# Performance work log

Hardware: AMD Instinct MI355X
Metric: run time of the kernel (lower is better)

Reference implementation:

```python
import jax, jax.numpy as jnp
import numpy as np

EPS = 1e-5  # torch BatchNorm1d default eps

# BinActive: sign forward, straight-through estimator backward (grad clipped where |x|>1)
@jax.custom_vjp
def bin_active(x):
    return jnp.sign(x)

def _ba_fwd(x):
    return jnp.sign(x), x

def _ba_bwd(x, g):
    return (g * (jnp.abs(x) <= 1.0).astype(g.dtype),)

bin_active.defvjp(_ba_fwd, _ba_bwd)

# XNOR-style weight binarization: sign(W) * mean(|W|) per output column, STE backward
@jax.custom_vjp
def bin_weight(w):
    alpha = jnp.mean(jnp.abs(w), axis=0, keepdims=True)  # [1, out]
    return jnp.sign(w) * alpha

def _bw_fwd(w):
    alpha = jnp.mean(jnp.abs(w), axis=0, keepdims=True)
    return jnp.sign(w) * alpha, w

def _bw_bwd(w, g):
    return (g * (jnp.abs(w) <= 1.0).astype(g.dtype),)

bin_weight.defvjp(_bw_fwd, _bw_bwd)


def setup_inputs() -> dict:
    key = jax.random.key(0)
    ks = jax.random.split(key, 8)
    N, E, IN, H, OUT = 100000, 1600000, 256, 128, 40
    x = jax.random.normal(ks[0], (N, IN), dtype=jnp.float32)
    edge_index = jax.random.randint(ks[1], (2, E), 0, N, dtype=jnp.int64)
    W0 = jax.random.normal(ks[2], (IN, H), dtype=jnp.float32) * (2.0 / IN) ** 0.5
    b0 = jnp.zeros((H,), dtype=jnp.float32)
    W1 = jax.random.normal(ks[3], (H, H), dtype=jnp.float32) * (2.0 / H) ** 0.5
    b1 = jnp.zeros((H,), dtype=jnp.float32)
    W2 = jax.random.normal(ks[4], (H, OUT), dtype=jnp.float32) * (2.0 / H) ** 0.5
    b2 = jnp.zeros((OUT,), dtype=jnp.float32)
    return {"x": x, "edge_index": edge_index, "W0": W0, "b0": b0,
            "W1": W1, "b1": b1, "W2": W2, "b2": b2}


def reference(x, edge_index, W0, b0, W1, b1, W2, b2):
    n = x.shape[0]
    loop = jnp.arange(n, dtype=edge_index.dtype)
    src = jnp.concatenate([edge_index[0], loop])  # add self loops (GCN norm)
    dst = jnp.concatenate([edge_index[1], loop])
    deg = jax.ops.segment_sum(jnp.ones_like(src, dtype=x.dtype), dst, num_segments=n)
    dinv = jnp.where(deg > 0, deg ** -0.5, 0.0)
    norm = (dinv[src] * dinv[dst])[:, None]  # [E+N, 1]

    # BatchNorm1d(affine=False), training-mode batch statistics (biased var)
    mu = jnp.mean(x, axis=0)
    var = jnp.var(x, axis=0)
    h = (x - mu) * jax.lax.rsqrt(var + EPS)

    for W, b in ((W0, b0), (W1, b1), (W2, b2)):
        h = bin_active(h)                       # sign binarize (dropout skipped: eval)
        h = h @ bin_weight(W)                   # binary-weight linear
        h = jax.ops.segment_sum(h[src] * norm, dst, num_segments=n) + b  # D^-1/2 (A+I) D^-1/2 agg
    return jax.nn.log_softmax(h, axis=1)
```

## Files before the change

### kernel.cpp

```cpp
#include <hip/hip_runtime.h>
#include <math.h>

#define IN_DIM 256
#define HD 128
#define OUT_DIM 40
#define S2_STRIDE 64
#define NB_CS 1024
#define NXCD 8
#define NCHUNK 64
#define NRANGE 4
#define RMAXW 6400

__device__ __forceinline__ int xcc_id() {
    int x;
    asm volatile("s_getreg_b32 %0, hwreg(HW_REG_XCC_ID)" : "=s"(x));
    return x & (NXCD - 1);
}

__device__ __forceinline__ void nt_load4(const int* p, int* o) {
    o[0] = __builtin_nontemporal_load(p + 0);
    o[1] = __builtin_nontemporal_load(p + 1);
    o[2] = __builtin_nontemporal_load(p + 2);
    o[3] = __builtin_nontemporal_load(p + 3);
}

__global__ __launch_bounds__(256) void k_init(float* muacc8) {
    int i = blockIdx.x * 256 + threadIdx.x;
    if (i < NXCD * 256) muacc8[i] = 0.f;
}

__global__ __launch_bounds__(256) void k_fuse1(const float* __restrict__ x, int N,
                                               float* __restrict__ muacc8,
                                               const int* __restrict__ ei, int E,
                                               unsigned char* __restrict__ cntC,
                                               const float* __restrict__ W0,
                                               const float* __restrict__ W1,
                                               const float* __restrict__ W2,
                                               unsigned long long* W0p,
                                               unsigned long long* W1p,
                                               unsigned long long* W2p,
                                               float* aS0, float* aS1, float* aS2) {
    __shared__ __align__(16) unsigned ldsbuf[RMAXW];
    int b = blockIdx.x, tid = threadIdx.x;
    if (b < NB_CS) {
        float* lds = (float*)ldsbuf;
        size_t F4 = (size_t)N * (IN_DIM / 4);
        size_t stride = (size_t)NB_CS * 256;
        float a0 = 0.f, a1 = 0.f, a2 = 0.f, a3 = 0.f;
        const float4* x4 = (const float4*)x;
        for (size_t i = (size_t)b * 256 + tid; i < F4; i += stride) {
            float4 v = x4[i];
            a0 += v.x; a1 += v.y; a2 += v.z; a3 += v.w;
        }
        lds[tid] = 0.f;
        __syncthreads();
        int c0 = (tid * 4) & 255;
        atomicAdd(&lds[c0], a0);
        atomicAdd(&lds[c0 + 1], a1);
        atomicAdd(&lds[c0 + 2], a2);
        atomicAdd(&lds[c0 + 3], a3);
        __syncthreads();
        int xc = xcc_id();
        __hip_atomic_fetch_add(&muacc8[xc * 256 + tid], lds[tid],
                               __ATOMIC_RELAXED, __HIP_MEMORY_SCOPE_WORKGROUP);
    } else if (b < NB_CS + NCHUNK * NRANGE) {
        int bid2 = b - NB_CS;
        int c = bid2 >> 2, r = bid2 & (NRANGE - 1);
        for (int i = tid; i < RMAXW; i += 256) ldsbuf[i] = 0u;
        __syncthreads();
        int R = (N + NRANGE - 1) / NRANGE;
        int base = r * R;
        int lim = N - base; if (lim > R) lim = R; if (lim < 0) lim = 0;
        int chunk = ((E + NCHUNK - 1) / NCHUNK + 3) & ~3;
        int eBeg = c * chunk, eEnd = E < eBeg + chunk ? E : eBeg + chunk;
        const int* dptr = ei + E;
        int e = eBeg;
        if ((((unsigned)(E + eBeg)) & 3u) == 0 && eBeg < eEnd) {
            int n4 = (eEnd - eBeg) >> 2;
            for (int i = tid; i < n4; i += 256) {
                int dd[4];
                nt_load4(dptr + eBeg + 4 * i, dd);
                unsigned r0 = (unsigned)(dd[0] - base);
                unsigned r1 = (unsigned)(dd[1] - base);
                unsigned r2 = (unsigned)(dd[2] - base);
                unsigned r3 = (unsigned)(dd[3] - base);
                if (r0 < (unsigned)lim) atomicAdd(&ldsbuf[r0 >> 2], 1u << (8 * (r0 & 3)));
                if (r1 < (unsigned)lim) atomicAdd(&ldsbuf[r1 >> 2], 1u << (8 * (r1 & 3)));
                if (r2 < (unsigned)lim) atomicAdd(&ldsbuf[r2 >> 2], 1u << (8 * (r2 & 3)));
                if (r3 < (unsigned)lim) atomicAdd(&ldsbuf[r3 >> 2], 1u << (8 * (r3 & 3)));
            }
            e = eBeg + (n4 << 2);
        }
        for (e += tid; e < eEnd; e += 256) {
            unsigned rel = (unsigned)(dptr[e] - base);
            if (rel < (unsigned)lim) atomicAdd(&ldsbuf[rel >> 2], 1u << (8 * (rel & 3)));
        }
        __syncthreads();
        for (int i = tid; i < lim; i += 256) {
            unsigned cv = (ldsbuf[i >> 2] >> (8 * (i & 3))) & 0xFFu;
            cntC[(size_t)c * N + base + i] = (unsigned char)cv;
        }
    } else {
        int b2 = b - NB_CS - NCHUNK * NRANGE;
        int lane = tid & 63, w = tid >> 6;
        if (b2 < 32) {
            int j = b2 * 4 + w;
            float asum = 0.f;
            unsigned long long words[4];
            #pragma unroll
            for (int q = 0; q < 4; ++q) {
                float v = W0[(size_t)(4 * lane + q) * HD + j];
                asum += fabsf(v);
                words[q] = __ballot(v < 0.f);
            }
            #pragma unroll
            for (int off = 32; off; off >>= 1) asum += __shfl_xor(asum, off);
            if (lane == 0) {
                aS0[j] = 2.f * asum / 256.f;
                #pragma unroll
                for (int q = 0; q < 4; ++q) W0p[j * 4 + q] = words[q];
            }
        } else if (b2 < 64) {
            int j = (b2 - 32) * 4 + w;
            float asum = 0.f;
            unsigned long long words[2];
            #pragma unroll
            for (int p = 0; p < 2; ++p) {
                float v = W1[(size_t)(2 * lane + p) * HD + j];
                asum += fabsf(v);
                words[p] = __ballot(v < 0.f);
            }
            #pragma unroll
            for (int off = 32; off; off >>= 1) asum += __shfl_xor(asum, off);
            if (lane == 0) {
                aS1[j] = 2.f * asum / 128.f;
                W1p[j * 2 + 0] = words[0];
                W1p[j * 2 + 1] = words[1];
            }
        } else {
            int j = (b2 - 64) * 4 + w;
            if (j < OUT_DIM) {
                float asum = 0.f;
                unsigned long long words[2];
                #pragma unroll
                for (int p = 0; p < 2; ++p) {
                    float v = W2[(size_t)(2 * lane + p) * OUT_DIM + j];
                    asum += fabsf(v);
                    words[p] = __ballot(v < 0.f);
                }
                #pragma unroll
                for (int off = 32; off; off >>= 1) asum += __shfl_xor(asum, off);
                if (lane == 0) {
                    aS2[j] = 2.f * asum / 128.f;
                    W2p[j * 2 + 0] = words[0];
                    W2p[j * 2 + 1] = words[1];
                }
            }
        }
    }
}

__global__ __launch_bounds__(256) void k_bp(unsigned char* __restrict__ cntC, int N,
                                            int* bp, float* __restrict__ dinv,
                                            int* __restrict__ cnt) {
    __shared__ int sm[256];
    int i = blockIdx.x * 256 + threadIdx.x;
    int c = 0;
    if (i < N) {
        int run = 0;
        #pragma unroll
        for (int h = 0; h < NCHUNK; ++h) {
            unsigned bc = cntC[(size_t)h * N + i];
            cntC[(size_t)h * N + i] = (unsigned char)run;
            run += (int)bc;
        }
        c = run;
        cnt[i] = run;
        dinv[i] = (float)(1.0 / sqrt((double)(run + 1)));
    }
    sm[threadIdx.x] = c;
    __syncthreads();
    for (int off = 128; off; off >>= 1) {
        if (threadIdx.x < off) sm[threadIdx.x] += sm[threadIdx.x + off];
        __syncthreads();
    }
    if (threadIdx.x == 0) bp[blockIdx.x] = sm[0];
}

__global__ __launch_bounds__(512) void k_scanbp(const int* __restrict__ bp, int NB, int* bps,
                                                const float* __restrict__ muacc8,
                                                float* __restrict__ mu) {
    __shared__ int sm[512];
    int t = threadIdx.x;
    if (t < 256) {
        float s = 0.f;
        #pragma unroll
        for (int xc = 0; xc < NXCD; ++xc) s += muacc8[xc * 256 + t];
        mu[t] = s;
    }
    int v = (t < NB) ? bp[t] : 0;
    sm[t] = v;
    __syncthreads();
    for (int off = 1; off < 512; off <<= 1) {
        int add = (t >= off) ? sm[t - off] : 0;
        __syncthreads();
        sm[t] += add;
        __syncthreads();
    }
    if (t < NB) bps[t] = sm[t] - v;
}

__global__ __launch_bounds__(256) void k_rowptr(const int* __restrict__ cnt,
                                                const int* __restrict__ bps, int N, int E,
                                                int* row_ptr) {
    __shared__ int wsum[4];
    int t = threadIdx.x, lane = t & 63, w = t >> 6;
    int i = blockIdx.x * 256 + t;
    int c = (i < N) ? cnt[i] : 0;
    int v = c;
    #pragma unroll
    for (int off = 1; off < 64; off <<= 1) {
        int n = __shfl_up(v, off);
        if (lane >= off) v += n;
    }
    if (lane == 63) wsum[w] = v;
    __syncthreads();
    int wo = 0;
    for (int k = 0; k < w; ++k) wo += wsum[k];
    int excl = bps[blockIdx.x] + wo + v - c;
    if (i < N) row_ptr[i] = excl;
    if (blockIdx.x == 0 && t == 0) row_ptr[N] = E;
}

__global__ __launch_bounds__(256) void k_fuse2(const int* __restrict__ ei, int E,
                                               const int* __restrict__ rowp,
                                               const unsigned char* __restrict__ xoffC,
                                               int* __restrict__ cs4,
                                               const float* __restrict__ x,
                                               const float* __restrict__ muacc, float inv_n,
                                               const unsigned long long* __restrict__ W0p,
                                               unsigned char* __restrict__ S0, int N) {
    __shared__ __align__(16) unsigned sh32[RMAXW];
    int b = blockIdx.x, tid = threadIdx.x;
    if (b < NCHUNK * NRANGE) {
        int c = b >> 2, r = b & (NRANGE - 1);
        for (int i = tid; i < RMAXW; i += 256) sh32[i] = 0u;
        __syncthreads();
        int R = (N + NRANGE - 1) / NRANGE;
        int base = r * R;
        int lim = N - base; if (lim > R) lim = R; if (lim < 0) lim = 0;
        int chunk = ((E + NCHUNK - 1) / NCHUNK + 3) & ~3;
        int eBeg = c * chunk, eEnd = E < eBeg + chunk ? E : eBeg + chunk;
        int e = eBeg;
        if (((unsigned)eBeg & 3u) == 0 && (((unsigned)(E + eBeg)) & 3u) == 0 && eBeg < eEnd) {
            int n4 = (eEnd - eBeg) >> 2;
            for (int i = tid; i < n4; i += 256) {
                int ss[4], dd[4];
                nt_load4(ei + eBeg + 4 * i, ss);
                nt_load4(ei + E + eBeg + 4 * i, dd);
                #pragma unroll
                for (int k = 0; k < 4; ++k) {
                    unsigned rel = (unsigned)(dd[k] - base);
                    if (rel < (unsigned)lim) {
                        unsigned old = atomicAdd(&sh32[rel >> 2], 1u << (8 * (rel & 3)));
                        int lr = (int)((old >> (8 * (rel & 3))) & 0xFFu);
                        int pos = rowp[dd[k]] +
                                  (int)xoffC[(size_t)c * N + dd[k]] + lr;
                        cs4[pos] = ss[k];
                    }
                }
            }
            e = eBeg + (n4 << 2);
        }
        for (e += tid; e < eEnd; e += 256) {
            int d = ei[E + e];
            unsigned rel = (unsigned)(d - base);
            if (rel < (unsigned)lim) {
                unsigned old = atomicAdd(&sh32[rel >> 2], 1u << (8 * (rel & 3)));
                int lr = (int)((old >> (8 * (rel & 3))) & 0xFFu);
                int pos = rowp[d] + (int)xoffC[(size_t)c * N + d] + lr;
                cs4[pos] = ei[e];
            }
        }
    } else {
        unsigned long long* w0s = (unsigned long long*)sh32;
        {
            int i = tid;
            w0s[9 * (i >> 3) + (i & 7)] = W0p[i];
            i = tid + 256;
            w0s[9 * (i >> 3) + (i & 7)] = W0p[i];
        }
        __syncthreads();
        int lane = tid & 63;
        int row = (b - NCHUNK * NRANGE) * 4 + (tid >> 6);
        if (row >= N) return;
        float4 xv = ((const float4*)(x + (size_t)row * IN_DIM))[lane];
        float4 ms = ((const float4*)muacc)[lane];
        unsigned long long xw[4];
        xw[0] = __ballot(xv.x < ms.x * inv_n);
        xw[1] = __ballot(xv.y < ms.y * inv_n);
        xw[2] = __ballot(xv.z < ms.z * inv_n);
        xw[3] = __ballot(xv.w < ms.w * inv_n);
        unsigned int pack = 0;
        #pragma unroll
        for (int t2 = 0; t2 < 2; ++t2) {
            const unsigned long long* wc = &w0s[9 * lane + 4 * t2];
            int dd = __popcll(xw[0] ^ wc[0]) + __popcll(xw[1] ^ wc[1]) +
                     __popcll(xw[2] ^ wc[2]) + __popcll(xw[3] ^ wc[3]);
            int S = IN_DIM - 2 * dd;
            int s8 = S >> 1;
            if (s8 > 127) s8 = 127;
            pack |= ((unsigned int)(s8 + 128) & 0xffu) << (8 * t2);
        }
        *(unsigned short*)(S0 + (size_t)row * HD + 2 * lane) = (unsigned short)pack;
    }
}

template <int OUTC>
__global__ __launch_bounds__(256) void k_agg_mm(const unsigned char* __restrict__ Sin,
                                                const int* __restrict__ row_ptr,
                                                const int* __restrict__ cs4,
                                                const float* __restrict__ dinv,
                                                const float* __restrict__ alphaS,
                                                const float* __restrict__ bias,
                                                const unsigned long long* __restrict__ Wnp,
                                                unsigned char* __restrict__ Sout, int N) {
    __shared__ unsigned long long wsm[OUTC * 2 + OUTC / 4 + 8];
    int tid = threadIdx.x;
    for (int i = tid; i < OUTC * 2; i += 256) wsm[9 * (i >> 3) + (i & 7)] = Wnp[i];
    __syncthreads();
    int lane = tid & 63;
    int d = blockIdx.x * 4 + (tid >> 6);
    if (d >= N) return;
    unsigned fo = (unsigned)lane * 2;
    float dv = dinv[d];
    float p0a[4] = {0.f, 0.f, 0.f, 0.f};
    float p1a[4] = {0.f, 0.f, 0.f, 0.f};
    {
        float nrm = dv * dv;
        unsigned v = *(const unsigned short*)(Sin + (((unsigned)d << 7) + fo));
        p0a[0] = fmaf(nrm, (float)(v & 0xffu) - 128.f, p0a[0]);
        p1a[0] = fmaf(nrm, (float)(v >> 8) - 128.f, p1a[0]);
    }
    int e0 = row_ptr[d], e1 = row_ptr[d + 1];
    int e = e0;
    for (; e + 7 < e1; e += 8) {
        int s[8]; float n[8]; unsigned v[8];
        #pragma unroll
        for (int j = 0; j < 8; ++j) s[j] = __builtin_nontemporal_load(&cs4[e + j]);
        #pragma unroll
        for (int j = 0; j < 8; ++j) n[j] = dinv[s[j]] * dv;
        #pragma unroll
        for (int j = 0; j < 8; ++j)
            v[j] = *(const unsigned short*)(Sin + (((unsigned)s[j] << 7) + fo));
        #pragma unroll
        for (int j = 0; j < 8; ++j) {
            p0a[j & 3] = fmaf(n[j], (float)(v[j] & 0xffu) - 128.f, p0a[j & 3]);
            p1a[j & 3] = fmaf(n[j], (float)(v[j] >> 8) - 128.f, p1a[j & 3]);
        }
    }
    for (int q = 0; e < e1; ++e, ++q) {
        int s = cs4[e];
        float nrm = dinv[s] * dv;
        unsigned v = *(const unsigned short*)(Sin + (((unsigned)s << 7) + fo));
        p0a[q & 3] = fmaf(nrm, (float)(v & 0xffu) - 128.f, p0a[q & 3]);
        p1a[q & 3] = fmaf(nrm, (float)(v >> 8) - 128.f, p1a[q & 3]);
    }
    float a0 = (p0a[0] + p0a[1]) + (p0a[2] + p0a[3]);
    float a1 = (p1a[0] + p1a[1]) + (p1a[2] + p1a[3]);
    float h0 = alphaS[fo] * a0 + bias[fo];
    float h1 = alphaS[fo + 1] * a1 + bias[fo + 1];
    unsigned long long x0 = __ballot(h0 < 0.f);
    unsigned long long x1 = __ballot(h1 < 0.f);
    if (OUTC == 128) {
        unsigned pack = 0;
        #pragma unroll
        for (int t2 = 0; t2 < 2; ++t2) {
            int j = 2 * lane + t2;
            int i0 = j * 2;
            const unsigned long long* wc = &wsm[9 * (i0 >> 3) + (i0 & 7)];
            int dd = __popcll(x0 ^ wc[0]) + __popcll(x1 ^ wc[1]);
            int S = HD - 2 * dd;
            pack |= ((unsigned)((S >> 1) + 128) & 0xffu) << (8 * t2);
        }
        *(unsigned short*)(Sout + (size_t)d * HD + fo) = (unsigned short)pack;
    } else {
        int p8 = 128;
        if (lane < OUTC) {
            int i0 = lane * 2;
            const unsigned long long* wc = &wsm[9 * (i0 >> 3) + (i0 & 7)];
            int dd = __popcll(x0 ^ wc[0]) + __popcll(x1 ^ wc[1]);
            p8 = ((HD - 2 * dd) >> 1) + 128;
        }
        Sout[(size_t)d * S2_STRIDE + lane] = (unsigned char)p8;
    }
}

__global__ __launch_bounds__(256) void k_agg_out(const unsigned char* __restrict__ S2,
                                                 const int* __restrict__ row_ptr,
                                                 const int* __restrict__ cs4,
                                                 const float* __restrict__ dinv,
                                                 const float* __restrict__ alphaS2,
                                                 const float* __restrict__ b2,
                                                 float* __restrict__ out, int N) {
    int tid = threadIdx.x, lane = tid & 63;
    int d = blockIdx.x * 4 + (tid >> 6);
    if (d >= N) return;
    float dv = dinv[d];
    float pa[4] = {0.f, 0.f, 0.f, 0.f};
    {
        float nrm = dv * dv;
        unsigned v = S2[((unsigned)d << 6) + lane];
        pa[0] = fmaf(nrm, (float)v - 128.f, pa[0]);
    }
    int e0 = row_ptr[d], e1 = row_ptr[d + 1];
    int e = e0;
    for (; e + 7 < e1; e += 8) {
        int s[8]; float n[8]; unsigned v[8];
        #pragma unroll
        for (int j = 0; j < 8; ++j) s[j] = __builtin_nontemporal_load(&cs4[e + j]);
        #pragma unroll
        for (int j = 0; j < 8; ++j) n[j] = dinv[s[j]] * dv;
        #pragma unroll
        for (int j = 0; j < 8; ++j) v[j] = S2[((unsigned)s[j] << 6) + lane];
        #pragma unroll
        for (int j = 0; j < 8; ++j) pa[j & 3] = fmaf(n[j], (float)v[j] - 128.f, pa[j & 3]);
    }
    for (int q = 0; e < e1; ++e, ++q) {
        int s = cs4[e];
        float nrm = dinv[s] * dv;
        unsigned v = S2[((unsigned)s << 6) + lane];
        pa[q & 3] = fmaf(nrm, (float)v - 128.f, pa[q & 3]);
    }
    float a0 = (pa[0] + pa[1]) + (pa[2] + pa[3]);
    float h = (lane < OUT_DIM) ? (alphaS2[lane] * a0 + b2[lane]) : -INFINITY;
    float mymax = h;
    #pragma unroll
    for (int off = 1; off < 64; off <<= 1) mymax = fmaxf(mymax, __shfl_xor(mymax, off));
    float s4 = (lane < OUT_DIM) ? expf(h - mymax) : 0.f;
    #pragma unroll
    for (int off = 1; off < 64; off <<= 1) s4 += __shfl_xor(s4, off);
    float lse = mymax + logf(s4);
    if (lane < OUT_DIM) out[(size_t)d * OUT_DIM + lane] = h - lse;
}

extern "C" void kernel_launch(void* const* d_in, const int* in_sizes, int n_in,
                              void* d_out, int out_size, void* d_ws, size_t ws_size,
                              hipStream_t stream) {
    const float* x  = (const float*)d_in[0];
    const int*   ei = (const int*)d_in[1];
    const float* W0 = (const float*)d_in[2];
    const float* b0 = (const float*)d_in[3];
    const float* W1 = (const float*)d_in[4];
    const float* b1 = (const float*)d_in[5];
    const float* W2 = (const float*)d_in[6];
    const float* b2 = (const float*)d_in[7];
    float* out = (float*)d_out;

    int N = in_sizes[0] / IN_DIM;
    int E = in_sizes[1] / 2;

    char* ws = (char*)d_ws;
    size_t off = 0;
    auto alloc = [&](size_t bytes) -> void* {
        off = (off + 255) & ~(size_t)255;
        void* p = (void*)(ws + off);
        off += bytes;
        return p;
    };
    float* mu     = (float*)alloc(256 * 4);
    float* muacc8 = (float*)alloc(NXCD * 256 * 4);
    unsigned char* cntC = (unsigned char*)alloc((size_t)NCHUNK * N);
    int*   cnt    = (int*)alloc((size_t)N * 4);
    float* dinv   = (float*)alloc((size_t)N * 4);
    int*   rowp   = (int*)alloc(((size_t)N + 1) * 4);
    int*   bp     = (int*)alloc(512 * 4);
    int*   bps    = (int*)alloc(512 * 4);
    int*   cs4    = (int*)alloc((size_t)E * 4);
    unsigned char* S0 = (unsigned char*)alloc((size_t)N * HD);
    unsigned char* S1 = (unsigned char*)alloc((size_t)N * HD);
    unsigned char* S2 = (unsigned char*)alloc((size_t)N * S2_STRIDE);
    unsigned long long* W0p = (unsigned long long*)alloc(128 * 4 * 8);
    unsigned long long* W1p = (unsigned long long*)alloc(128 * 2 * 8);
    unsigned long long* W2p = (unsigned long long*)alloc(40 * 2 * 8);
    float* aS0 = (float*)alloc(128 * 4);
    float* aS1 = (float*)alloc(128 * 4);
    float* aS2 = (float*)alloc(40 * 4);

    int nb256 = (N + 255) / 256;
    float inv_n = 1.0f / (float)N;

    k_init<<<dim3(8), dim3(256), 0, stream>>>(muacc8);
    k_fuse1<<<dim3(NB_CS + NCHUNK * NRANGE + 74), dim3(256), 0, stream>>>(
        x, N, muacc8, ei, E, cntC, W0, W1, W2, W0p, W1p, W2p, aS0, aS1, aS2);
    k_bp<<<dim3(nb256), dim3(256), 0, stream>>>(cntC, N, bp, dinv, cnt);
    k_scanbp<<<dim3(1), dim3(512), 0, stream>>>(bp, nb256, bps, muacc8, mu);
    k_rowptr<<<dim3(nb256), dim3(256), 0, stream>>>(cnt, bps, N, E, rowp);

    int nb4 = (N + 3) / 4;
    k_fuse2<<<dim3(NCHUNK * NRANGE + nb4), dim3(256), 0, stream>>>(
        ei, E, rowp, cntC, cs4, x, mu, inv_n, W0p, S0, N);
    k_agg_mm<128><<<dim3(nb4), dim3(256), 0, stream>>>(S0, rowp, cs4, dinv, aS0, b0, W1p, S1, N);
    k_agg_mm<40><<<dim3(nb4), dim3(256), 0, stream>>>(S1, rowp, cs4, dinv, aS1, b1, W2p, S2, N);
    k_agg_out<<<dim3(nb4), dim3(256), 0, stream>>>(S2, rowp, cs4, dinv, aS2, b2, out, N);
    (void)out_size; (void)ws_size; (void)n_in;
}
```

Before: 536.2 us.

## Split aggregation wave across edges with 16-byte row loads and shuffle reduction

The aggregation kernels now assign sub-groups of lanes to different edges. In the hidden layers, 8 edge slots of 8 lanes each load 16-byte chunks of int8 rows. In the output layer, 16 slots of 4 lanes each do the same. Partial sums are then reduced across slots with shuffles. Previously every lane read 2 bytes per edge in a sequential edge loop. The sign bits are rebuilt through per-bit ballots, and the weight packing order in k_fuse1 is permuted to match the new feature-to-lane mapping. The aim is fewer, wider gathers and more edges in flight per wave, at the cost of 16 accumulators per lane plus extra shuffle and ballot work.

```diff
diff --git a/kernel.cpp b/kernel.cpp
--- a/kernel.cpp
+++ b/kernel.cpp
@@ -22,6 +22,18 @@
     o[1] = __builtin_nontemporal_load(p + 1);
     o[2] = __builtin_nontemporal_load(p + 2);
     o[3] = __builtin_nontemporal_load(p + 3);
+}
+
+__device__ __forceinline__ void addrow16(float n, uint4 r, float* acc) {
+    unsigned w[4] = {r.x, r.y, r.z, r.w};
+    #pragma unroll
+    for (int q = 0; q < 4; ++q) {
+        unsigned v = w[q];
+        acc[4 * q + 0] = fmaf(n, (float)(v & 0xffu) - 128.f, acc[4 * q + 0]);
+        acc[4 * q + 1] = fmaf(n, (float)((v >> 8) & 0xffu) - 128.f, acc[4 * q + 1]);
+        acc[4 * q + 2] = fmaf(n, (float)((v >> 16) & 0xffu) - 128.f, acc[4 * q + 2]);
+        acc[4 * q + 3] = fmaf(n, (float)(v >> 24) - 128.f, acc[4 * q + 3]);
+    }
 }
 
 __global__ __launch_bounds__(256) void k_init(float* muacc8) {
@@ -122,11 +134,12 @@
             }
         } else if (b2 < 64) {
             int j = (b2 - 32) * 4 + w;
+            int row0 = (lane & 7) * 16 + (lane >> 3);
             float asum = 0.f;
             unsigned long long words[2];
             #pragma unroll
             for (int p = 0; p < 2; ++p) {
-                float v = W1[(size_t)(2 * lane + p) * HD + j];
+                float v = W1[(size_t)(row0 + 8 * p) * HD + j];
                 asum += fabsf(v);
                 words[p] = __ballot(v < 0.f);
             }
@@ -139,12 +152,13 @@
             }
         } else {
             int j = (b2 - 64) * 4 + w;
+            int row0 = (lane & 7) * 16 + (lane >> 3);
             if (j < OUT_DIM) {
                 float asum = 0.f;
                 unsigned long long words[2];
                 #pragma unroll
                 for (int p = 0; p < 2; ++p) {
-                    float v = W2[(size_t)(2 * lane + p) * OUT_DIM + j];
+                    float v = W2[(size_t)(row0 + 8 * p) * OUT_DIM + j];
                     asum += fabsf(v);
                     words[p] = __ballot(v < 0.f);
                 }
@@ -332,46 +346,53 @@
     int lane = tid & 63;
     int d = blockIdx.x * 4 + (tid >> 6);
     if (d >= N) return;
-    unsigned fo = (unsigned)lane * 2;
+    int slot = lane >> 3;
+    unsigned fo = ((unsigned)lane & 7) * 16;
     float dv = dinv[d];
-    float p0a[4] = {0.f, 0.f, 0.f, 0.f};
-    float p1a[4] = {0.f, 0.f, 0.f, 0.f};
-    {
+    float acc[16];
+    #pragma unroll
+    for (int k = 0; k < 16; ++k) acc[k] = 0.f;
+    if (slot == 0) {
         float nrm = dv * dv;
-        unsigned v = *(const unsigned short*)(Sin + (((unsigned)d << 7) + fo));
-        p0a[0] = fmaf(nrm, (float)(v & 0xffu) - 128.f, p0a[0]);
-        p1a[0] = fmaf(nrm, (float)(v >> 8) - 128.f, p1a[0]);
+        uint4 r = *(const uint4*)(Sin + (((size_t)d) << 7) + fo);
+        addrow16(nrm, r, acc);
     }
     int e0 = row_ptr[d], e1 = row_ptr[d + 1];
-    int e = e0;
-    for (; e + 7 < e1; e += 8) {
-        int s[8]; float n[8]; unsigned v[8];
-        #pragma unroll
-        for (int j = 0; j < 8; ++j) s[j] = __builtin_nontemporal_load(&cs4[e + j]);
-        #pragma unroll
-        for (int j = 0; j < 8; ++j) n[j] = dinv[s[j]] * dv;
-        #pragma unroll
-        for (int j = 0; j < 8; ++j)
-            v[j] = *(const unsigned short*)(Sin + (((unsigned)s[j] << 7) + fo));
-        #pragma unroll
-        for (int j = 0; j < 8; ++j) {
-            p0a[j & 3] = fmaf(n[j], (float)(v[j] & 0xffu) - 128.f, p0a[j & 3]);
-            p1a[j & 3] = fmaf(n[j], (float)(v[j] >> 8) - 128.f, p1a[j & 3]);
-        }
-    }
-    for (int q = 0; e < e1; ++e, ++q) {
+    int e = e0 + slot;
+    for (; e + 8 < e1; e += 16) {
+        int sA = cs4[e], sB = cs4[e + 8];
+        float nA = dinv[sA] * dv, nB = dinv[sB] * dv;
+        uint4 rA = *(const uint4*)(Sin + (((size_t)sA) << 7) + fo);
+        uint4 rB = *(const uint4*)(Sin + (((size_t)sB) << 7) + fo);
+        addrow16(nA, rA, acc);
+        addrow16(nB, rB, acc);
+    }
+    if (e < e1) {
         int s = cs4[e];
         float nrm = dinv[s] * dv;
-        unsigned v = *(const unsigned short*)(Sin + (((unsigned)s << 7) + fo));
-        p0a[q & 3] = fmaf(nrm, (float)(v & 0xffu) - 128.f, p0a[q & 3]);
-        p1a[q & 3] = fmaf(nrm, (float)(v >> 8) - 128.f, p1a[q & 3]);
-    }
-    float a0 = (p0a[0] + p0a[1]) + (p0a[2] + p0a[3]);
-    float a1 = (p1a[0] + p1a[1]) + (p1a[2] + p1a[3]);
-    float h0 = alphaS[fo] * a0 + bias[fo];
-    float h1 = alphaS[fo + 1] * a1 + bias[fo + 1];
-    unsigned long long x0 = __ballot(h0 < 0.f);
-    unsigned long long x1 = __ballot(h1 < 0.f);
+        uint4 r = *(const uint4*)(Sin + (((size_t)s) << 7) + fo);
+        addrow16(nrm, r, acc);
+    }
+    #pragma unroll
+    for (int k = 0; k < 16; ++k) {
+        acc[k] += __shfl_xor(acc[k], 8);
+        acc[k] += __shfl_xor(acc[k], 16);
+        acc[k] += __shfl_xor(acc[k], 32);
+    }
+    unsigned m16 = 0;
+    #pragma unroll
+    for (int k = 0; k < 16; ++k) {
+        float hv = alphaS[fo + k] * acc[k] + bias[fo + k];
+        if (hv < 0.f) m16 |= (1u << k);
+    }
+    unsigned long long x0 = 0, x1 = 0;
+    #pragma unroll
+    for (int k = 0; k < 8; ++k) {
+        unsigned long long b0 = __ballot((m16 >> k) & 1u);
+        unsigned long long b1 = __ballot((m16 >> (k + 8)) & 1u);
+        x0 |= (b0 & 0xffULL) << (8 * k);
+        x1 |= (b1 & 0xffULL) << (8 * k);
+    }
     if (OUTC == 128) {
         unsigned pack = 0;
         #pragma unroll
@@ -383,7 +404,7 @@
             int S = HD - 2 * dd;
             pack |= ((unsigned)((S >> 1) + 128) & 0xffu) << (8 * t2);
         }
-        *(unsigned short*)(Sout + (size_t)d * HD + fo) = (unsigned short)pack;
+        *(unsigned short*)(Sout + (size_t)d * HD + 2 * lane) = (unsigned short)pack;
     } else {
         int p8 = 128;
         if (lane < OUTC) {
@@ -406,42 +427,74 @@
     int tid = threadIdx.x, lane = tid & 63;
     int d = blockIdx.x * 4 + (tid >> 6);
     if (d >= N) return;
+    int slot = lane >> 2;
+    int u = lane & 3;
+    unsigned fo = (unsigned)u * 16;
     float dv = dinv[d];
-    float pa[4] = {0.f, 0.f, 0.f, 0.f};
-    {
+    float acc[16];
+    #pragma unroll
+    for (int k = 0; k < 16; ++k) acc[k] = 0.f;
+    if (slot == 0) {
         float nrm = dv * dv;
-        unsigned v = S2[((unsigned)d << 6) + lane];
-        pa[0] = fmaf(nrm, (float)v - 128.f, pa[0]);
+        uint4 r = *(const uint4*)(S2 + (((size_t)d) << 6) + fo);
+        addrow16(nrm, r, acc);
     }
     int e0 = row_ptr[d], e1 = row_ptr[d + 1];
-    int e = e0;
-    for (; e + 7 < e1; e += 8) {
-        int s[8]; float n[8]; unsigned v[8];
-        #pragma unroll
-        for (int j = 0; j < 8; ++j) s[j] = __builtin_nontemporal_load(&cs4[e + j]);
-        #pragma unroll
-        for (int j = 0; j < 8; ++j) n[j] = dinv[s[j]] * dv;
-        #pragma unroll
-        for (int j = 0; j < 8; ++j) v[j] = S2[((unsigned)s[j] << 6) + lane];
-        #pragma unroll
-        for (int j = 0; j < 8; ++j) pa[j & 3] = fmaf(n[j], (float)v[j] - 128.f, pa[j & 3]);
-    }
-    for (int q = 0; e < e1; ++e, ++q) {
+    int e = e0 + slot;
+    for (; e + 16 < e1; e += 32) {
+        int sA = cs4[e], sB = cs4[e + 16];
+        float nA = dinv[sA] * dv, nB = dinv[sB] * dv;
+        uint4 rA = *(const uint4*)(S2 + (((size_t)sA) << 6) + fo);
+        uint4 rB = *(const uint4*)(S2 + (((size_t)sB) << 6) + fo);
+        addrow16(nA, rA, acc);
+        addrow16(nB, rB, acc);
+    }
+    if (e < e1) {
         int s = cs4[e];
         float nrm = dinv[s] * dv;
-        unsigned v = S2[((unsigned)s << 6) + lane];
-        pa[q & 3] = fmaf(nrm, (float)v - 128.f, pa[q & 3]);
-    }
-    float a0 = (pa[0] + pa[1]) + (pa[2] + pa[3]);
-    float h = (lane < OUT_DIM) ? (alphaS2[lane] * a0 + b2[lane]) : -INFINITY;
-    float mymax = h;
-    #pragma unroll
-    for (int off = 1; off < 64; off <<= 1) mymax = fmaxf(mymax, __shfl_xor(mymax, off));
-    float s4 = (lane < OUT_DIM) ? expf(h - mymax) : 0.f;
-    #pragma unroll
-    for (int off = 1; off < 64; off <<= 1) s4 += __shfl_xor(s4, off);
+        uint4 r = *(const uint4*)(S2 + (((size_t)s) << 6) + fo);
+        addrow16(nrm, r, acc);
+    }
+    #pragma unroll
+    for (int k = 0; k < 16; ++k) {
+        acc[k] += __shfl_xor(acc[k], 4);
+        acc[k] += __shfl_xor(acc[k], 8);
+        acc[k] += __shfl_xor(acc[k], 16);
+        acc[k] += __shfl_xor(acc[k], 32);
+    }
+    float h[16];
+    float mymax = -INFINITY;
+    #pragma unroll
+    for (int k = 0; k < 16; ++k) {
+        int f = (int)fo + k;
+        h[k] = (f < OUT_DIM) ? (alphaS2[f] * acc[k] + b2[f]) : -INFINITY;
+        mymax = fmaxf(mymax, h[k]);
+    }
+    mymax = fmaxf(mymax, __shfl_xor(mymax, 1));
+    mymax = fmaxf(mymax, __shfl_xor(mymax, 2));
+    float s4 = 0.f;
+    #pragma unroll
+    for (int k = 0; k < 16; ++k) {
+        if ((int)fo + k < OUT_DIM) s4 += expf(h[k] - mymax);
+    }
+    s4 += __shfl_xor(s4, 1);
+    s4 += __shfl_xor(s4, 2);
     float lse = mymax + logf(s4);
-    if (lane < OUT_DIM) out[(size_t)d * OUT_DIM + lane] = h - lse;
+    if (slot == 0) {
+        float* op = out + (size_t)d * OUT_DIM + fo;
+        #pragma unroll
+        for (int qw = 0; qw < 4; ++qw) {
+            int f = (int)fo + 4 * qw;
+            if (f < OUT_DIM) {
+                float4 o;
+                o.x = h[4 * qw + 0] - lse;
+                o.y = h[4 * qw + 1] - lse;
+                o.z = h[4 * qw + 2] - lse;
+                o.w = h[4 * qw + 3] - lse;
+                *(float4*)(op + 4 * qw) = o;
+            }
+        }
+    }
 }
 
 extern "C" void kernel_launch(void* const* d_in, const int* in_sizes, int n_in,
```

Result: slower. 604.7 us (+12.8%).
